# Performance work log

Measured on AMD Instinct MI355X. Metric: run time of the kernel, lower is better.

The kernel has to match this reference:

```python
import jax, jax.numpy as jnp
import numpy as np

B, S, D, H = 4, 2048, 1024, 16
DK = D // H


def setup_inputs() -> dict:
    key = jax.random.key(0)
    ks = jax.random.split(key, 8)
    scale = 1.0 / np.sqrt(D)
    return {
        "q": jax.random.normal(ks[0], (B, S, D), jnp.float32),
        "k": jax.random.normal(ks[1], (B, S, D), jnp.float32),
        "v": jax.random.normal(ks[2], (B, S, D), jnp.float32),
        "mask": jnp.ones((1,), jnp.int32),  # unused (original code never applies it)
        "W_Q": jax.random.normal(ks[3], (D, D), jnp.float32) * scale,
        "W_K": jax.random.normal(ks[4], (D, D), jnp.float32) * scale,
        "W_V": jax.random.normal(ks[5], (D, D), jnp.float32) * scale,
        "W_O": jax.random.normal(ks[6], (D, D), jnp.float32) * scale,
    }


def reference(q, k, v, mask, W_Q, W_K, W_V, W_O):
    # nn.Linear(bias=False): y = x @ W.T ; weight shape [out, in]
    query = q @ W_Q.T  # [B,S,D]
    key_ = k @ W_K.T
    value = v @ W_V.T
    # split heads -> [B,H,S,DK]
    query = query.reshape(B, S, H, DK).transpose(0, 2, 1, 3)
    key_ = key_.reshape(B, S, H, DK).transpose(0, 2, 1, 3)
    value = value.reshape(B, S, H, DK).transpose(0, 2, 1, 3)
    # naive attention: full [B,H,S,S] score matrix (faithful to source)
    scores = jnp.einsum("bhqd,bhkd->bhqk", query, key_) / jnp.sqrt(
        jnp.asarray(DK, query.dtype)
    )
    attn = jax.nn.softmax(scores, axis=-1)  # dropout p=0.0 -> identity
    x = jnp.einsum("bhqk,bhkd->bhqd", attn, value)  # [B,H,S,DK]
    x = x.transpose(0, 2, 1, 3).reshape(B, S, D)
    return x @ W_O.T
```

## Files before the change

kernel.cpp:

```cpp
#include <hip/hip_runtime.h>
#include <math.h>


#define DEV __device__ __forceinline__

typedef __bf16 bf16x8 __attribute__((ext_vector_type(8)));
typedef __bf16 bf16x2 __attribute__((ext_vector_type(2)));
typedef float f32x4 __attribute__((ext_vector_type(4)));
typedef unsigned int u32x2 __attribute__((ext_vector_type(2)));

typedef __attribute__((address_space(1))) const unsigned int g_u32;
typedef __attribute__((address_space(3))) unsigned int l_u32;

DEV unsigned short f2bf(float x) {
  unsigned int u = __float_as_uint(x);
  u += 0x7fffu + ((u >> 16) & 1u);
  return (unsigned short)(u >> 16);
}

DEV unsigned int pack2bf(float a, float b) {
#if __has_builtin(__builtin_amdgcn_cvt_pk_bf16_f32)
  bf16x2 r = __builtin_amdgcn_cvt_pk_bf16_f32(a, b);
  union { bf16x2 v; unsigned int u; } c;
  c.v = r;
  return c.u;
#else
  unsigned int ua = __float_as_uint(a) + 0x8000u;
  unsigned int ub = __float_as_uint(b) + 0x8000u;
  return (ua >> 16) | (ub & 0xffff0000u);
#endif
}

DEV float fexp2(float x) {
#if __has_builtin(__builtin_amdgcn_exp2f)
  return __builtin_amdgcn_exp2f(x);
#else
  return __expf(x * 0.69314718056f);
#endif
}

DEV void ld16(const unsigned short* g, unsigned short* l) {
  __builtin_amdgcn_global_load_lds((g_u32*)g, (l_u32*)l, 16, 0, 0);
}

__global__ __launch_bounds__(256) void cast_all(
    const float* __restrict__ q, const float* __restrict__ k,
    const float* __restrict__ v, const float* __restrict__ w0,
    const float* __restrict__ w1, const float* __restrict__ w2,
    const float* __restrict__ w3, unsigned short* __restrict__ qb,
    unsigned short* __restrict__ kb, unsigned short* __restrict__ vb,
    unsigned short* __restrict__ o0, unsigned short* __restrict__ o1,
    unsigned short* __restrict__ o2, unsigned short* __restrict__ o3) {
  const int bb = blockIdx.x;
  const float* src;
  unsigned short* dst;
  int i;
  if (bb < 24576) {
    const int z = bb >> 13, lb = bb & 8191;
    src = (z == 0) ? q : (z == 1) ? k : v;
    dst = (z == 0) ? qb : (z == 1) ? kb : vb;
    i = lb * 256 + threadIdx.x;
  } else {
    const int t = bb - 24576;
    const int z = t >> 10, lb = t & 1023;
    src = (z == 0) ? w0 : (z == 1) ? w1 : (z == 2) ? w2 : w3;
    dst = (z == 0) ? o0 : (z == 1) ? o1 : (z == 2) ? o2 : o3;
    i = lb * 256 + threadIdx.x;
  }
  float4 vv = reinterpret_cast<const float4*>(src)[i];
  ushort4 o;
  o.x = f2bf(vv.x); o.y = f2bf(vv.y); o.z = f2bf(vv.z); o.w = f2bf(vv.w);
  reinterpret_cast<ushort4*>(dst)[i] = o;
}

template <bool SW>
DEV void gemm_core(const unsigned short* __restrict__ A,
                   const unsigned short* __restrict__ W,
                   unsigned short* As, unsigned short* Bs,
                   f32x4 (&acc)[4][4], int tileM, int tileN) {
  const int tid = threadIdx.x;
  const int w = tid >> 6, lane = tid & 63;
  const int wr = (w & 1) * 64, wc = (w >> 1) * 64;
  const int l15 = lane & 15, g4 = lane >> 4, l7 = l15 & 7;
  const int rsub = lane >> 3;
  const int gsrc = (lane & 7) ^ rsub;

  const f32x4 fzero = {0.f, 0.f, 0.f, 0.f};
#pragma unroll
  for (int i = 0; i < 4; i++)
#pragma unroll
    for (int j = 0; j < 4; j++) acc[i][j] = fzero;

  for (int k0 = 0; k0 < 1024; k0 += 64) {
#pragma unroll
    for (int j = 0; j < 4; ++j) {
      const int c = w * 4 + j;
      ld16(A + (size_t)(tileM + c * 8 + rsub) * 1024 + k0 + gsrc * 8, As + c * 512);
      ld16(W + (size_t)(tileN + c * 8 + rsub) * 1024 + k0 + gsrc * 8, Bs + c * 512);
    }
    __syncthreads();
#pragma unroll
    for (int kc = 0; kc < 2; kc++) {
      const int ph = ((kc * 4 + g4) ^ l7) * 8;
      bf16x8 aF[4], bF[4];
#pragma unroll
      for (int i = 0; i < 4; i++)
        aF[i] = *reinterpret_cast<const bf16x8*>(&As[(wr + i * 16 + l15) * 64 + ph]);
#pragma unroll
      for (int j = 0; j < 4; j++)
        bF[j] = *reinterpret_cast<const bf16x8*>(&Bs[(wc + j * 16 + l15) * 64 + ph]);
#pragma unroll
      for (int i = 0; i < 4; i++)
#pragma unroll
        for (int j = 0; j < 4; j++) {
          if (SW)
            acc[j][i] = __builtin_amdgcn_mfma_f32_16x16x32_bf16(bF[j], aF[i], acc[j][i], 0, 0, 0);
          else
            acc[i][j] = __builtin_amdgcn_mfma_f32_16x16x32_bf16(aF[i], bF[j], acc[i][j], 0, 0, 0);
        }
    }
    __syncthreads();
  }
}

__global__ __launch_bounds__(256) void gemm_qkv(
    const unsigned short* __restrict__ qb, const unsigned short* __restrict__ kb,
    const unsigned short* __restrict__ vb, const unsigned short* __restrict__ Wq,
    const unsigned short* __restrict__ Wk, const unsigned short* __restrict__ Wv,
    unsigned short* __restrict__ Qp, unsigned short* __restrict__ Kp,
    unsigned short* __restrict__ VpT) {
  __shared__ __align__(16) unsigned short As[128 * 64];
  __shared__ __align__(16) unsigned short Bs[128 * 64];
  const int z = blockIdx.z;
  const int tileM = blockIdx.x * 128, tileN = blockIdx.y * 128;
  const int tid = threadIdx.x, w = tid >> 6, lane = tid & 63;
  const int wr = (w & 1) * 64, wc = (w >> 1) * 64;
  const int l15 = lane & 15, g4 = lane >> 4;
  f32x4 acc[4][4];

  if (z < 2) {
    gemm_core<true>((z == 0) ? qb : kb, (z == 0) ? Wq : Wk, As, Bs, acc, tileM, tileN);
    const float qs = (z == 0) ? 0.125f * 1.44269504089f : 1.0f;
    unsigned short* C = (z == 0) ? Qp : Kp;
#pragma unroll
    for (int i = 0; i < 4; i++) {
      const size_t row = (size_t)(tileM + wr + i * 16 + l15);
#pragma unroll
      for (int j = 0; j < 4; j++) {
        const int col = tileN + wc + j * 16 + g4 * 4;
        ushort4 pk;
        pk.x = f2bf(acc[j][i][0] * qs); pk.y = f2bf(acc[j][i][1] * qs);
        pk.z = f2bf(acc[j][i][2] * qs); pk.w = f2bf(acc[j][i][3] * qs);
        *reinterpret_cast<ushort4*>(&C[row * 1024 + col]) = pk;
      }
    }
  } else {
    gemm_core<false>(vb, Wv, As, Bs, acc, tileM, tileN);
    const int b = tileM / 2048, s0 = tileM % 2048;
#pragma unroll
    for (int i = 0; i < 4; i++)
#pragma unroll
      for (int j = 0; j < 4; j++) {
        int col = tileN + wc + j * 16 + l15;
        int s = s0 + wr + i * 16 + g4 * 4;
        ushort4 pk;
        pk.x = f2bf(acc[i][j][0]); pk.y = f2bf(acc[i][j][1]);
        pk.z = f2bf(acc[i][j][2]); pk.w = f2bf(acc[i][j][3]);
        *reinterpret_cast<ushort4*>(&VpT[(size_t)(b * 1024 + col) * 2048 + s]) = pk;
      }
  }
}

__global__ __launch_bounds__(256) void gemm_out(
    const unsigned short* __restrict__ Xp, const unsigned short* __restrict__ Wo,
    float* __restrict__ out) {
  __shared__ __align__(16) unsigned short As[128 * 64];
  __shared__ __align__(16) unsigned short Bs[128 * 64];
  const int tileM = blockIdx.x * 128, tileN = blockIdx.y * 128;
  f32x4 acc[4][4];
  gemm_core<true>(Xp, Wo, As, Bs, acc, tileM, tileN);
  const int tid = threadIdx.x, w = tid >> 6, lane = tid & 63;
  const int wr = (w & 1) * 64, wc = (w >> 1) * 64;
  const int l15 = lane & 15, g4 = lane >> 4;
#pragma unroll
  for (int i = 0; i < 4; i++) {
    const size_t row = (size_t)(tileM + wr + i * 16 + l15);
#pragma unroll
    for (int j = 0; j < 4; j++) {
      const int col = tileN + wc + j * 16 + g4 * 4;
      *reinterpret_cast<f32x4*>(&out[row * 1024 + col]) = acc[j][i];
    }
  }
}

__global__ __launch_bounds__(256, 4) void attn(
    const unsigned short* __restrict__ Qp, const unsigned short* __restrict__ Kp,
    const unsigned short* __restrict__ VpT, unsigned short* __restrict__ Xp) {
  __shared__ __align__(16) unsigned short Ks[2 * 64 * 64];
  __shared__ __align__(16) unsigned short Vs[2 * 64 * 64];
  __shared__ __align__(16) unsigned short Ps[4 * 16 * 64];

  const int bid = blockIdx.x;
  const int nid = (bid & 7) * 128 + (bid >> 3);
  const int qt = nid & 15, bh = nid >> 4;
  const int b = bh >> 4, h = bh & 15;
  const int q0 = qt * 128;
  const int tid = threadIdx.x, w = tid >> 6, lane = tid & 63;
  const int l15 = lane & 15, g4 = lane >> 4;
  const int l7 = l15 & 7;

  const int rsub = lane >> 3;
  const int gsrc = (lane & 7) ^ rsub;

  bf16x8 qf[2][2];
#pragma unroll
  for (int mi = 0; mi < 2; mi++) {
    const unsigned short* Qrow =
        Qp + (size_t)(b * 2048 + q0 + w * 32 + mi * 16 + l15) * 1024 + h * 64;
    qf[mi][0] = *reinterpret_cast<const bf16x8*>(Qrow + g4 * 8);
    qf[mi][1] = *reinterpret_cast<const bf16x8*>(Qrow + 32 + g4 * 8);
  }

  const f32x4 fzero = {0.f, 0.f, 0.f, 0.f};
  f32x4 o[2][4];
#pragma unroll
  for (int mi = 0; mi < 2; mi++)
#pragma unroll
    for (int dj = 0; dj < 4; dj++) o[mi][dj] = fzero;
  float l_i[2] = {0.f, 0.f};

  const unsigned short* Kbase = Kp + (size_t)(b * 2048) * 1024 + h * 64;
  const unsigned short* Vbase = VpT + (size_t)(b * 1024 + h * 64) * 2048;
  unsigned short* Pw = Ps + w * 1024;

  const int c = w * 2;

#pragma unroll
  for (int j = 0; j < 2; ++j) {
    ld16(Kbase + (size_t)((c + j) * 8 + rsub) * 1024 + gsrc * 8, Ks + (c + j) * 512);
    ld16(Vbase + (size_t)((c + j) * 8 + rsub) * 2048 + gsrc * 8, Vs + (c + j) * 512);
  }
  __syncthreads();

  int cur = 0;
  for (int t = 0; t < 32; ++t) {
    const int kt = t * 64;
    unsigned short* Kc = Ks + cur * 4096;
    unsigned short* Vc = Vs + cur * 4096;

    if (t < 31) {
      unsigned short* Kn = Ks + (cur ^ 1) * 4096;
      unsigned short* Vn = Vs + (cur ^ 1) * 4096;
      const int ktn = kt + 64;
#pragma unroll
      for (int j = 0; j < 2; ++j) {
        ld16(Kbase + (size_t)(ktn + (c + j) * 8 + rsub) * 1024 + gsrc * 8,
             Kn + (c + j) * 512);
        ld16(Vbase + (size_t)((c + j) * 8 + rsub) * 2048 + ktn + gsrc * 8,
             Vn + (c + j) * 512);
      }
    }

    f32x4 sv[2][4];
    __builtin_amdgcn_s_setprio(1);
#pragma unroll
    for (int jt = 0; jt < 4; jt++) {
      const int row = jt * 16 + l15;
      const int s0 = g4 ^ l7;
      bf16x8 kf0 = *reinterpret_cast<const bf16x8*>(&Kc[row * 64 + s0 * 8]);
      bf16x8 kf1 = *reinterpret_cast<const bf16x8*>(&Kc[row * 64 + (s0 ^ 4) * 8]);
#pragma unroll
      for (int mi = 0; mi < 2; mi++) {
        f32x4 z = fzero;
        z = __builtin_amdgcn_mfma_f32_16x16x32_bf16(kf0, qf[mi][0], z, 0, 0, 0);
        z = __builtin_amdgcn_mfma_f32_16x16x32_bf16(kf1, qf[mi][1], z, 0, 0, 0);
        sv[mi][jt] = z;
      }
    }
    __builtin_amdgcn_s_setprio(0);

#pragma unroll
    for (int mi = 0; mi < 2; mi++) {
      float rs = 0.f;
#pragma unroll
      for (int jt = 0; jt < 4; jt++)
#pragma unroll
        for (int r = 0; r < 4; r++) {
          sv[mi][jt][r] = fexp2(sv[mi][jt][r]);
          rs += sv[mi][jt][r];
        }
      l_i[mi] += rs;
    }

    bf16x8 vf[2][4];
#pragma unroll
    for (int kc = 0; kc < 2; kc++)
#pragma unroll
      for (int dj = 0; dj < 4; dj++)
        vf[kc][dj] = *reinterpret_cast<const bf16x8*>(
            &Vc[(dj * 16 + l15) * 64 + ((kc * 4 + g4) ^ l7) * 8]);

#pragma unroll
    for (int mi = 0; mi < 2; mi++) {
#pragma unroll
      for (int jt = 0; jt < 4; jt++) {
        u32x2 pk;
        pk.x = pack2bf(sv[mi][jt][0], sv[mi][jt][1]);
        pk.y = pack2bf(sv[mi][jt][2], sv[mi][jt][3]);
        const int slot = (jt * 4 + g4) ^ l15;
        *reinterpret_cast<u32x2*>(&Pw[l15 * 64 + slot * 4]) = pk;
      }
      __builtin_amdgcn_s_setprio(1);
#pragma unroll
      for (int kc = 0; kc < 2; kc++) {
        const int sA = (kc * 8 + g4 * 2) ^ l15;
        const int sB = (kc * 8 + g4 * 2 + 1) ^ l15;
        u32x2 pa = *reinterpret_cast<const u32x2*>(&Pw[l15 * 64 + sA * 4]);
        u32x2 pb = *reinterpret_cast<const u32x2*>(&Pw[l15 * 64 + sB * 4]);
        union { unsigned int u[4]; bf16x8 v; } pf;
        pf.u[0] = pa.x; pf.u[1] = pa.y; pf.u[2] = pb.x; pf.u[3] = pb.y;
#pragma unroll
        for (int dj = 0; dj < 4; dj++)
          o[mi][dj] = __builtin_amdgcn_mfma_f32_16x16x32_bf16(vf[kc][dj], pf.v,
                                                             o[mi][dj], 0, 0, 0);
      }
      __builtin_amdgcn_s_setprio(0);
    }

    __syncthreads();
    cur ^= 1;
  }

#pragma unroll
  for (int mi = 0; mi < 2; mi++) {
    float rs = l_i[mi];
    rs += __shfl_xor(rs, 16);
    rs += __shfl_xor(rs, 32);
    const float inv = 1.f / rs;
    const size_t row = (size_t)(b * 2048 + q0 + w * 32 + mi * 16 + l15);
#pragma unroll
    for (int dj = 0; dj < 4; dj++) {
      ushort4 pk;
      pk.x = f2bf(o[mi][dj][0] * inv);
      pk.y = f2bf(o[mi][dj][1] * inv);
      pk.z = f2bf(o[mi][dj][2] * inv);
      pk.w = f2bf(o[mi][dj][3] * inv);
      *reinterpret_cast<ushort4*>(&Xp[row * 1024 + h * 64 + dj * 16 + g4 * 4]) = pk;
    }
  }
}

extern "C" void kernel_launch(void* const* d_in, const int* in_sizes, int n_in,
                              void* d_out, int out_size, void* d_ws, size_t ws_size,
                              hipStream_t stream) {
  const float* q  = (const float*)d_in[0];
  const float* k  = (const float*)d_in[1];
  const float* v  = (const float*)d_in[2];
  const float* Wq = (const float*)d_in[4];
  const float* Wk = (const float*)d_in[5];
  const float* Wv = (const float*)d_in[6];
  const float* Wo = (const float*)d_in[7];
  float* out = (float*)d_out;

  char* ws = (char*)d_ws;
  const size_t MB = 1u << 20;
  unsigned short* qb  = (unsigned short*)(ws + 0 * MB);
  unsigned short* kb  = (unsigned short*)(ws + 16 * MB);
  unsigned short* vb  = (unsigned short*)(ws + 32 * MB);
  unsigned short* wqb = (unsigned short*)(ws + 48 * MB);
  unsigned short* wkb = (unsigned short*)(ws + 50 * MB);
  unsigned short* wvb = (unsigned short*)(ws + 52 * MB);
  unsigned short* wob = (unsigned short*)(ws + 54 * MB);
  unsigned short* Qp  = (unsigned short*)(ws + 56 * MB);
  unsigned short* Kp  = (unsigned short*)(ws + 72 * MB);
  unsigned short* VpT = (unsigned short*)(ws + 88 * MB);
  unsigned short* Xp  = (unsigned short*)(ws + 104 * MB);

  cast_all<<<dim3(28672), 256, 0, stream>>>(q, k, v, Wq, Wk, Wv, Wo,
                                            qb, kb, vb, wqb, wkb, wvb, wob);

  dim3 gq(64, 8, 3);
  gemm_qkv<<<gq, 256, 0, stream>>>(qb, kb, vb, wqb, wkb, wvb, Qp, Kp, VpT);

  attn<<<dim3(1024), 256, 0, stream>>>(Qp, Kp, VpT, Xp);

  dim3 go(64, 8, 1);
  gemm_out<<<go, 256, 0, stream>>>(Xp, wob, out);
}
```

Baseline: 365.6 us.

## Software-pipeline attention loop: overlap QK^T of next tile with PV of previous

Restructures the attention main loop into a prologue, steady state and epilogue. Each iteration computes QK^T for tile t and PV for tile t-1, with the P fragments carried in registers across iterations. The goal is to let the exp/softmax VALU work overlap with MFMA work and to issue loads for the next tile after the first barrier. The cost is more live registers, an extra barrier per iteration, and V buffer reuse timing that has to be right.

```diff
diff --git a/kernel.cpp b/kernel.cpp
--- a/kernel.cpp
+++ b/kernel.cpp
@@ -235,6 +235,8 @@
 
   const int c = w * 2;
 
+  u32x2 pfa[2][2], pfb[2][2];
+
 #pragma unroll
   for (int j = 0; j < 2; ++j) {
     ld16(Kbase + (size_t)((c + j) * 8 + rsub) * 1024 + gsrc * 8, Ks + (c + j) * 512);
@@ -242,33 +244,22 @@
   }
   __syncthreads();
 
-  int cur = 0;
-  for (int t = 0; t < 32; ++t) {
-    const int kt = t * 64;
-    unsigned short* Kc = Ks + cur * 4096;
-    unsigned short* Vc = Vs + cur * 4096;
-
-    if (t < 31) {
-      unsigned short* Kn = Ks + (cur ^ 1) * 4096;
-      unsigned short* Vn = Vs + (cur ^ 1) * 4096;
-      const int ktn = kt + 64;
-#pragma unroll
-      for (int j = 0; j < 2; ++j) {
-        ld16(Kbase + (size_t)(ktn + (c + j) * 8 + rsub) * 1024 + gsrc * 8,
-             Kn + (c + j) * 512);
-        ld16(Vbase + (size_t)((c + j) * 8 + rsub) * 2048 + ktn + gsrc * 8,
-             Vn + (c + j) * 512);
-      }
-    }
-
+  {
+#pragma unroll
+    for (int j = 0; j < 2; ++j) {
+      ld16(Kbase + (size_t)(64 + (c + j) * 8 + rsub) * 1024 + gsrc * 8,
+           Ks + 4096 + (c + j) * 512);
+      ld16(Vbase + (size_t)((c + j) * 8 + rsub) * 2048 + 64 + gsrc * 8,
+           Vs + 4096 + (c + j) * 512);
+    }
     f32x4 sv[2][4];
     __builtin_amdgcn_s_setprio(1);
 #pragma unroll
     for (int jt = 0; jt < 4; jt++) {
       const int row = jt * 16 + l15;
       const int s0 = g4 ^ l7;
-      bf16x8 kf0 = *reinterpret_cast<const bf16x8*>(&Kc[row * 64 + s0 * 8]);
-      bf16x8 kf1 = *reinterpret_cast<const bf16x8*>(&Kc[row * 64 + (s0 ^ 4) * 8]);
+      bf16x8 kf0 = *reinterpret_cast<const bf16x8*>(&Ks[row * 64 + s0 * 8]);
+      bf16x8 kf1 = *reinterpret_cast<const bf16x8*>(&Ks[row * 64 + (s0 ^ 4) * 8]);
 #pragma unroll
       for (int mi = 0; mi < 2; mi++) {
         f32x4 z = fzero;
@@ -278,7 +269,6 @@
       }
     }
     __builtin_amdgcn_s_setprio(0);
-
 #pragma unroll
     for (int mi = 0; mi < 2; mi++) {
       float rs = 0.f;
@@ -291,15 +281,6 @@
         }
       l_i[mi] += rs;
     }
-
-    bf16x8 vf[2][4];
-#pragma unroll
-    for (int kc = 0; kc < 2; kc++)
-#pragma unroll
-      for (int dj = 0; dj < 4; dj++)
-        vf[kc][dj] = *reinterpret_cast<const bf16x8*>(
-            &Vc[(dj * 16 + l15) * 64 + ((kc * 4 + g4) ^ l7) * 8]);
-
 #pragma unroll
     for (int mi = 0; mi < 2; mi++) {
 #pragma unroll
@@ -310,25 +291,133 @@
         const int slot = (jt * 4 + g4) ^ l15;
         *reinterpret_cast<u32x2*>(&Pw[l15 * 64 + slot * 4]) = pk;
       }
-      __builtin_amdgcn_s_setprio(1);
 #pragma unroll
       for (int kc = 0; kc < 2; kc++) {
         const int sA = (kc * 8 + g4 * 2) ^ l15;
         const int sB = (kc * 8 + g4 * 2 + 1) ^ l15;
-        u32x2 pa = *reinterpret_cast<const u32x2*>(&Pw[l15 * 64 + sA * 4]);
-        u32x2 pb = *reinterpret_cast<const u32x2*>(&Pw[l15 * 64 + sB * 4]);
+        pfa[mi][kc] = *reinterpret_cast<const u32x2*>(&Pw[l15 * 64 + sA * 4]);
+        pfb[mi][kc] = *reinterpret_cast<const u32x2*>(&Pw[l15 * 64 + sB * 4]);
+      }
+    }
+    __syncthreads();
+  }
+
+  int cur = 1;
+  for (int t = 1; t < 32; ++t) {
+    unsigned short* Kc = Ks + cur * 4096;
+    unsigned short* Vp = Vs + (cur ^ 1) * 4096;
+
+    f32x4 sv[2][4];
+    __builtin_amdgcn_s_setprio(1);
+#pragma unroll
+    for (int jt = 0; jt < 4; jt++) {
+      const int row = jt * 16 + l15;
+      const int s0 = g4 ^ l7;
+      bf16x8 kf0 = *reinterpret_cast<const bf16x8*>(&Kc[row * 64 + s0 * 8]);
+      bf16x8 kf1 = *reinterpret_cast<const bf16x8*>(&Kc[row * 64 + (s0 ^ 4) * 8]);
+#pragma unroll
+      for (int mi = 0; mi < 2; mi++) {
+        f32x4 z = fzero;
+        z = __builtin_amdgcn_mfma_f32_16x16x32_bf16(kf0, qf[mi][0], z, 0, 0, 0);
+        z = __builtin_amdgcn_mfma_f32_16x16x32_bf16(kf1, qf[mi][1], z, 0, 0, 0);
+        sv[mi][jt] = z;
+      }
+    }
+
+    bf16x8 vf[2][4];
+#pragma unroll
+    for (int kc = 0; kc < 2; kc++)
+#pragma unroll
+      for (int dj = 0; dj < 4; dj++)
+        vf[kc][dj] = *reinterpret_cast<const bf16x8*>(
+            &Vp[(dj * 16 + l15) * 64 + ((kc * 4 + g4) ^ l7) * 8]);
+
+#pragma unroll
+    for (int mi = 0; mi < 2; mi++)
+#pragma unroll
+      for (int kc = 0; kc < 2; kc++) {
         union { unsigned int u[4]; bf16x8 v; } pf;
-        pf.u[0] = pa.x; pf.u[1] = pa.y; pf.u[2] = pb.x; pf.u[3] = pb.y;
+        pf.u[0] = pfa[mi][kc].x; pf.u[1] = pfa[mi][kc].y;
+        pf.u[2] = pfb[mi][kc].x; pf.u[3] = pfb[mi][kc].y;
 #pragma unroll
         for (int dj = 0; dj < 4; dj++)
           o[mi][dj] = __builtin_amdgcn_mfma_f32_16x16x32_bf16(vf[kc][dj], pf.v,
                                                              o[mi][dj], 0, 0, 0);
       }
-      __builtin_amdgcn_s_setprio(0);
+    __builtin_amdgcn_s_setprio(0);
+
+    __syncthreads();
+
+    if (t < 31) {
+      unsigned short* Kn = Ks + (cur ^ 1) * 4096;
+      unsigned short* Vn = Vs + (cur ^ 1) * 4096;
+      const int ktn = (t + 1) * 64;
+#pragma unroll
+      for (int j = 0; j < 2; ++j) {
+        ld16(Kbase + (size_t)(ktn + (c + j) * 8 + rsub) * 1024 + gsrc * 8,
+             Kn + (c + j) * 512);
+        ld16(Vbase + (size_t)((c + j) * 8 + rsub) * 2048 + ktn + gsrc * 8,
+             Vn + (c + j) * 512);
+      }
+    }
+
+#pragma unroll
+    for (int mi = 0; mi < 2; mi++) {
+      float rs = 0.f;
+#pragma unroll
+      for (int jt = 0; jt < 4; jt++)
+#pragma unroll
+        for (int r = 0; r < 4; r++) {
+          sv[mi][jt][r] = fexp2(sv[mi][jt][r]);
+          rs += sv[mi][jt][r];
+        }
+      l_i[mi] += rs;
+    }
+
+#pragma unroll
+    for (int mi = 0; mi < 2; mi++) {
+#pragma unroll
+      for (int jt = 0; jt < 4; jt++) {
+        u32x2 pk;
+        pk.x = pack2bf(sv[mi][jt][0], sv[mi][jt][1]);
+        pk.y = pack2bf(sv[mi][jt][2], sv[mi][jt][3]);
+        const int slot = (jt * 4 + g4) ^ l15;
+        *reinterpret_cast<u32x2*>(&Pw[l15 * 64 + slot * 4]) = pk;
+      }
+#pragma unroll
+      for (int kc = 0; kc < 2; kc++) {
+        const int sA = (kc * 8 + g4 * 2) ^ l15;
+        const int sB = (kc * 8 + g4 * 2 + 1) ^ l15;
+        pfa[mi][kc] = *reinterpret_cast<const u32x2*>(&Pw[l15 * 64 + sA * 4]);
+        pfb[mi][kc] = *reinterpret_cast<const u32x2*>(&Pw[l15 * 64 + sB * 4]);
+      }
     }
 
     __syncthreads();
     cur ^= 1;
+  }
+
+  {
+    unsigned short* Vp = Vs + (cur ^ 1) * 4096;
+    bf16x8 vf[2][4];
+#pragma unroll
+    for (int kc = 0; kc < 2; kc++)
+#pragma unroll
+      for (int dj = 0; dj < 4; dj++)
+        vf[kc][dj] = *reinterpret_cast<const bf16x8*>(
+            &Vp[(dj * 16 + l15) * 64 + ((kc * 4 + g4) ^ l7) * 8]);
+#pragma unroll
+    for (int mi = 0; mi < 2; mi++)
+#pragma unroll
+      for (int kc = 0; kc < 2; kc++) {
+        union { unsigned int u[4]; bf16x8 v; } pf;
+        pf.u[0] = pfa[mi][kc].x; pf.u[1] = pfa[mi][kc].y;
+        pf.u[2] = pfb[mi][kc].x; pf.u[3] = pfb[mi][kc].y;
+#pragma unroll
+        for (int dj = 0; dj < 4; dj++)
+          o[mi][dj] = __builtin_amdgcn_mfma_f32_16x16x32_bf16(vf[kc][dj], pf.v,
+                                                             o[mi][dj], 0, 0, 0);
+      }
   }
 
 #pragma unroll
```

New measurement: 358.9 us. About the same (-1.8%).
